# Performance work log

Measured on AMD Instinct MI355X. Metric: run time of the kernel, lower is better.

Reference implementation:

```python
import jax, jax.numpy as jnp
import numpy as np


def setup_inputs() -> dict:
    key = jax.random.key(0)
    kq, kk, kv = jax.random.split(key, 3)
    B, L, S, H, E = 2, 2048, 2048, 8, 64
    queries = jax.random.normal(kq, (B, L, H, E), dtype=jnp.float32)
    keys = jax.random.normal(kk, (B, S, H, E), dtype=jnp.float32)
    values = jax.random.normal(kv, (B, S, H, E), dtype=jnp.float32)
    a1 = jnp.float32(1.0)
    a2 = jnp.float32(1.0)
    return {"queries": queries, "keys": keys, "values": values, "a1": a1, "a2": a2}


def reference(queries, keys, values, a1, a2):
    # queries: (B,L,H,E); keys/values: (B,S,H,E)
    E = queries.shape[-1]
    scale = 1.0 / jnp.sqrt(jnp.float32(E))
    # shared QK scores: (B,H,L,S)
    qk = jnp.einsum('blhe,bshe->bhls', queries, keys) * scale
    # sparse branch: relu^2 (dropout = identity in eval)
    ssa = jnp.square(jax.nn.relu(qk))
    ssa_out = jnp.einsum('bhls,bshd->blhd', ssa, values)
    # dense branch: softmax over keys
    dsa = jax.nn.softmax(qk, axis=-1)
    dsa_out = jnp.einsum('bhls,bshd->blhd', dsa, values)
    w1 = jnp.exp(a1)
    w2 = jnp.exp(a2)
    alpha1 = w1 / (w1 + w2)
    alpha2 = w2 / (w1 + w2)
    return alpha1 * ssa_out + alpha2 * dsa_out
```

## Files before the change

### kernel.cpp

```cpp
#include <hip/hip_runtime.h>

typedef short short4v __attribute__((ext_vector_type(4)));
typedef short short8v __attribute__((ext_vector_type(8)));
typedef float float4v __attribute__((ext_vector_type(4)));
typedef unsigned short u16;

#define NB 2
#define NL 2048
#define NS 2048
#define NH 8
#define NE 64
#define HE (NH*NE)
#define NLT (NL/64)
#define NST (NS/64)
#define TILE_U16 4096

static __device__ __forceinline__ unsigned pk2bf(float a, float b) {
  union { float f; unsigned u; } x, y; x.f = a; y.f = b;
  return __builtin_amdgcn_perm(y.u + 0x8000u, x.u + 0x8000u, 0x07060302u);
}

#define GLD16(gp, lp) __builtin_amdgcn_global_load_lds( \
    (const __attribute__((address_space(1))) void*)(gp), \
    (__attribute__((address_space(3))) void*)(lp), 16, 0, 0)

static __device__ __forceinline__ int fK(int s) { return (s & 3) | ((s >> 1) & 4); }

__global__ __launch_bounds__(256)
void prepack(const float* __restrict__ kp, const float* __restrict__ vp,
             u16* __restrict__ kimg, u16* __restrict__ vimg)
{
  __shared__ __align__(16) u16 ldsv[TILE_U16];

  const int bid  = blockIdx.x;
  const int tile = bid >> 1;
  const int doV  = bid & 1;
  const int st = tile & (NST - 1);
  const int bh = tile >> 5;
  const int h  = bh & (NH - 1);
  const int b  = bh >> 3;
  const int s0 = st * 64;
  const size_t base = (size_t)b * NS * HE + h * NE;
  const int tid  = threadIdx.x;
  const int wv   = tid >> 6;
  const int lane = tid & 63;
  const int ln7  = lane & 7;

  if (!doV) {
    u16* kt = kimg + (size_t)tile * TILE_U16;
    for (int slot = tid; slot < 512; slot += 256) {
      const int srow = slot >> 3, p = slot & 7, c = p ^ fK(srow);
      const float* src = kp + base + (size_t)(s0 + srow) * HE + c * 8;
      float4 x0 = *(const float4*)src;
      float4 x1 = *(const float4*)(src + 4);
      unsigned d[4] = { pk2bf(x0.x, x0.y), pk2bf(x0.z, x0.w),
                        pk2bf(x1.x, x1.y), pk2bf(x1.z, x1.w) };
      *(int4*)(kt + slot * 8) = *(const int4*)d;
    }
    return;
  }

  u16* vt = vimg + (size_t)tile * TILE_U16;
  {
    const float* vcol = vp + base + (size_t)(s0 + wv * 16) * HE + lane;
    unsigned vr[8];
    #pragma unroll
    for (int jj = 0; jj < 8; ++jj)
      vr[jj] = pk2bf(vcol[(size_t)(2 * jj) * HE], vcol[(size_t)(2 * jj + 1) * HE]);
    #pragma unroll
    for (int i = 0; i < 2; ++i) {
      const int cs = (2 * wv + i) ^ ln7;
      int4 t4 = make_int4((int)vr[4*i+0], (int)vr[4*i+1],
                          (int)vr[4*i+2], (int)vr[4*i+3]);
      *(int4*)(&ldsv[lane * 64 + cs * 8]) = t4;
    }
  }
  __syncthreads();
  {
    const int4* s = (const int4*)ldsv;
    int4* dst = (int4*)vt;
    dst[tid]       = s[tid];
    dst[tid + 256] = s[tid + 256];
  }
}

__global__ __launch_bounds__(256, 2)
void assa_fwd(const float* __restrict__ qp, const u16* __restrict__ kimg,
              const u16* __restrict__ vimg, const float* __restrict__ a1p,
              const float* __restrict__ a2p, float* __restrict__ op)
{
  __shared__ __align__(16) u16 ldsb[2][2 * TILE_U16];

  const int tid  = threadIdx.x;
  const int wv   = tid >> 6;
  const int lane = tid & 63;
  const int ln15 = lane & 15;
  const int ln7  = lane & 7;
  const int quad = lane >> 4;

  const int bid = blockIdx.x;
  const int bh  = bid & 15;
  const int lt  = bid >> 4;
  const int h   = bh & (NH - 1);
  const int b   = bh >> 3;

  const int lbase = lt * 64 + wv * 16;

  short8v qf0, qf1;
  {
    const float* qrow = qp + ((size_t)(b * NL + lbase + ln15)) * HE + h * NE + quad * 8;
    float4 q0 = *(const float4*)(qrow);
    float4 q1 = *(const float4*)(qrow + 4);
    float4 q2 = *(const float4*)(qrow + 32);
    float4 q3 = *(const float4*)(qrow + 36);
    unsigned d0[4] = { pk2bf(0.125f*q0.x, 0.125f*q0.y), pk2bf(0.125f*q0.z, 0.125f*q0.w),
                       pk2bf(0.125f*q1.x, 0.125f*q1.y), pk2bf(0.125f*q1.z, 0.125f*q1.w) };
    unsigned d1[4] = { pk2bf(0.125f*q2.x, 0.125f*q2.y), pk2bf(0.125f*q2.z, 0.125f*q2.w),
                       pk2bf(0.125f*q3.x, 0.125f*q3.y), pk2bf(0.125f*q3.z, 0.125f*q3.w) };
    qf0 = *(const short8v*)d0;
    qf1 = *(const short8v*)d1;
  }

  short8v ones8;
  #pragma unroll
  for (int j = 0; j < 8; ++j) ones8[j] = (short)0x3F80;

  const size_t tbase = (size_t)bh * NST;

  float4v acc_s[4], acc_d[4], acc_l;
  #pragma unroll
  for (int t = 0; t < 4; ++t)
    #pragma unroll
    for (int r = 0; r < 4; ++r) { acc_s[t][r] = 0.0f; acc_d[t][r] = 0.0f; }
  #pragma unroll
  for (int r = 0; r < 4; ++r) acc_l[r] = 0.0f;

  auto dma_tile = [&](int st, int nb) {
    const int hf = wv & 1;
    const u16* g;
    u16* l;
    if (wv < 2) {
      g = kimg + (tbase + st) * TILE_U16 + hf * 2048 + lane * 8;
      l = &ldsb[nb][hf * 2048];
    } else {
      g = vimg + (tbase + st) * TILE_U16 + hf * 2048 + lane * 8;
      l = &ldsb[nb][TILE_U16 + hf * 2048];
    }
    GLD16(g,        l);
    GLD16(g +  512, l +  512);
    GLD16(g + 1024, l + 1024);
    GLD16(g + 1536, l + 1536);
  };

  dma_tile(0, 0);

  const int rperm = 8 * (ln15 >> 2) + (ln15 & 3);
  const int fk    = (ln15 & 3) | (((ln15 >> 2) & 1) << 2);

  for (int st = 0; st < NST; ++st) {
    __builtin_amdgcn_s_waitcnt(0);
    __syncthreads();
    if (st + 1 < NST) dma_tile(st + 1, (st + 1) & 1);

    const u16* kb_l = ldsb[st & 1];
    const u16* vb_l = ldsb[st & 1] + TILE_U16;

    #pragma unroll
    for (int U = 0; U < 2; ++U) {
      float4v sa0, sa1;
      #pragma unroll
      for (int r = 0; r < 4; ++r) { sa0[r] = 0.0f; sa1[r] = 0.0f; }
      const u16* krow0 = &kb_l[(32 * U + rperm) * 64];
      const u16* krow1 = krow0 + 4 * 64;
      short8v kf00 = *(const short8v*)(krow0 + (quad ^ fk) * 8);
      short8v kf01 = *(const short8v*)(krow0 + ((4 + quad) ^ fk) * 8);
      short8v kf10 = *(const short8v*)(krow1 + (quad ^ fk) * 8);
      short8v kf11 = *(const short8v*)(krow1 + ((4 + quad) ^ fk) * 8);
      sa0 = __builtin_amdgcn_mfma_f32_16x16x32_bf16(kf00, qf0, sa0, 0, 0, 0);
      sa0 = __builtin_amdgcn_mfma_f32_16x16x32_bf16(kf01, qf1, sa0, 0, 0, 0);
      sa1 = __builtin_amdgcn_mfma_f32_16x16x32_bf16(kf10, qf0, sa1, 0, 0, 0);
      sa1 = __builtin_amdgcn_mfma_f32_16x16x32_bf16(kf11, qf1, sa1, 0, 0, 0);

      float ps[8], pd[8];
      #pragma unroll
      for (int r = 0; r < 4; ++r) {
        float s0 = sa0[r], s1 = sa1[r];
        float r0 = s0 > 0.0f ? s0 : 0.0f;
        float r1 = s1 > 0.0f ? s1 : 0.0f;
        ps[r] = r0 * r0;  ps[4 + r] = r1 * r1;
        pd[r] = __expf(s0); pd[4 + r] = __expf(s1);
      }
      unsigned da[4] = { pk2bf(ps[0], ps[1]), pk2bf(ps[2], ps[3]),
                         pk2bf(ps[4], ps[5]), pk2bf(ps[6], ps[7]) };
      unsigned db[4] = { pk2bf(pd[0], pd[1]), pk2bf(pd[2], pd[3]),
                         pk2bf(pd[4], pd[5]), pk2bf(pd[6], pd[7]) };
      short8v as8 = *(const short8v*)da;
      short8v ad8 = *(const short8v*)db;

      acc_l = __builtin_amdgcn_mfma_f32_16x16x32_bf16(ad8, ones8, acc_l, 0, 0, 0);

      #pragma unroll
      for (int t = 0; t < 4; ++t) {
        short8v vf = *(const short8v*)(&vb_l[(t * 16 + ln15) * 64 +
                        (((4 * U + quad) ^ ln7) * 8)]);
        acc_s[t] = __builtin_amdgcn_mfma_f32_16x16x32_bf16(as8, vf, acc_s[t], 0, 0, 0);
        acc_d[t] = __builtin_amdgcn_mfma_f32_16x16x32_bf16(ad8, vf, acc_d[t], 0, 0, 0);
      }
    }
  }

  const float w1 = __expf(a1p[0]), w2 = __expf(a2p[0]);
  const float al1 = w1 / (w1 + w2);
  const float al2 = w2 / (w1 + w2);

  float c_d[4];
  #pragma unroll
  for (int r = 0; r < 4; ++r) c_d[r] = al2 / acc_l[r];

  #pragma unroll
  for (int t = 0; t < 4; ++t) {
    #pragma unroll
    for (int r = 0; r < 4; ++r) {
      float val = al1 * acc_s[t][r] + c_d[r] * acc_d[t][r];
      const int l = lbase + quad * 4 + r;
      const int e = t * 16 + ln15;
      op[((size_t)(b * NL + l)) * HE + h * NE + e] = val;
    }
  }
}

extern "C" void kernel_launch(void* const* d_in, const int* in_sizes, int n_in,
                              void* d_out, int out_size, void* d_ws, size_t ws_size,
                              hipStream_t stream) {
  const float* q  = (const float*)d_in[0];
  const float* k  = (const float*)d_in[1];
  const float* v  = (const float*)d_in[2];
  const float* a1 = (const float*)d_in[3];
  const float* a2 = (const float*)d_in[4];
  float* out = (float*)d_out;
  (void)in_sizes; (void)n_in; (void)out_size; (void)ws_size;

  u16* kimg = (u16*)d_ws;
  u16* vimg = kimg + (size_t)NB * NH * NST * TILE_U16;

  prepack<<<dim3(NB * NH * NST * 2), dim3(256), 0, stream>>>(k, v, kimg, vimg);
  assa_fwd<<<dim3(NB * NH * NLT), dim3(256), 0, stream>>>(q, kimg, vimg, a1, a2, out);
}
```

Before: 111.7 us.

## Fuse K/V bf16 conversion into attention kernel, drop prepack pass

Removes the separate prepack kernel that converted K and V to swizzled bf16 images in workspace. The main kernel now loads fp32 K/V directly into registers one tile ahead, converts and writes them (V transposed) into single-buffered LDS each iteration. This saves a kernel launch and the workspace write/read round trip. In exchange, every L-tile block re-reads and re-converts fp32 K/V (twice the bytes of bf16). The loop also gains an extra barrier and strided scalar V loads, replacing the async global-to-LDS DMA double buffering.

Result: slower. 115.4 us (+3.4%).

```diff
diff --git a/kernel.cpp b/kernel.cpp
--- a/kernel.cpp
+++ b/kernel.cpp
@@ -13,83 +13,21 @@
 #define HE (NH*NE)
 #define NLT (NL/64)
 #define NST (NS/64)
-#define TILE_U16 4096
 
 static __device__ __forceinline__ unsigned pk2bf(float a, float b) {
   union { float f; unsigned u; } x, y; x.f = a; y.f = b;
   return __builtin_amdgcn_perm(y.u + 0x8000u, x.u + 0x8000u, 0x07060302u);
 }
 
-#define GLD16(gp, lp) __builtin_amdgcn_global_load_lds( \
-    (const __attribute__((address_space(1))) void*)(gp), \
-    (__attribute__((address_space(3))) void*)(lp), 16, 0, 0)
-
 static __device__ __forceinline__ int fK(int s) { return (s & 3) | ((s >> 1) & 4); }
 
-__global__ __launch_bounds__(256)
-void prepack(const float* __restrict__ kp, const float* __restrict__ vp,
-             u16* __restrict__ kimg, u16* __restrict__ vimg)
-{
-  __shared__ __align__(16) u16 ldsv[TILE_U16];
-
-  const int bid  = blockIdx.x;
-  const int tile = bid >> 1;
-  const int doV  = bid & 1;
-  const int st = tile & (NST - 1);
-  const int bh = tile >> 5;
-  const int h  = bh & (NH - 1);
-  const int b  = bh >> 3;
-  const int s0 = st * 64;
-  const size_t base = (size_t)b * NS * HE + h * NE;
-  const int tid  = threadIdx.x;
-  const int wv   = tid >> 6;
-  const int lane = tid & 63;
-  const int ln7  = lane & 7;
-
-  if (!doV) {
-    u16* kt = kimg + (size_t)tile * TILE_U16;
-    for (int slot = tid; slot < 512; slot += 256) {
-      const int srow = slot >> 3, p = slot & 7, c = p ^ fK(srow);
-      const float* src = kp + base + (size_t)(s0 + srow) * HE + c * 8;
-      float4 x0 = *(const float4*)src;
-      float4 x1 = *(const float4*)(src + 4);
-      unsigned d[4] = { pk2bf(x0.x, x0.y), pk2bf(x0.z, x0.w),
-                        pk2bf(x1.x, x1.y), pk2bf(x1.z, x1.w) };
-      *(int4*)(kt + slot * 8) = *(const int4*)d;
-    }
-    return;
-  }
-
-  u16* vt = vimg + (size_t)tile * TILE_U16;
-  {
-    const float* vcol = vp + base + (size_t)(s0 + wv * 16) * HE + lane;
-    unsigned vr[8];
-    #pragma unroll
-    for (int jj = 0; jj < 8; ++jj)
-      vr[jj] = pk2bf(vcol[(size_t)(2 * jj) * HE], vcol[(size_t)(2 * jj + 1) * HE]);
-    #pragma unroll
-    for (int i = 0; i < 2; ++i) {
-      const int cs = (2 * wv + i) ^ ln7;
-      int4 t4 = make_int4((int)vr[4*i+0], (int)vr[4*i+1],
-                          (int)vr[4*i+2], (int)vr[4*i+3]);
-      *(int4*)(&ldsv[lane * 64 + cs * 8]) = t4;
-    }
-  }
-  __syncthreads();
-  {
-    const int4* s = (const int4*)ldsv;
-    int4* dst = (int4*)vt;
-    dst[tid]       = s[tid];
-    dst[tid + 256] = s[tid + 256];
-  }
-}
-
 __global__ __launch_bounds__(256, 2)
-void assa_fwd(const float* __restrict__ qp, const u16* __restrict__ kimg,
-              const u16* __restrict__ vimg, const float* __restrict__ a1p,
+void assa_fwd(const float* __restrict__ qp, const float* __restrict__ kp,
+              const float* __restrict__ vp, const float* __restrict__ a1p,
               const float* __restrict__ a2p, float* __restrict__ op)
 {
-  __shared__ __align__(16) u16 ldsb[2][2 * TILE_U16];
+  __shared__ __align__(16) u16 lds_k[64 * 64];
+  __shared__ __align__(16) u16 lds_vt[64 * 64];
 
   const int tid  = threadIdx.x;
   const int wv   = tid >> 6;
@@ -125,7 +63,30 @@
   #pragma unroll
   for (int j = 0; j < 8; ++j) ones8[j] = (short)0x3F80;
 
-  const size_t tbase = (size_t)bh * NST;
+  const size_t kvb = (size_t)b * NS * HE + h * NE;
+  const float* kb = kp + kvb;
+  const float* vb = vp + kvb;
+
+  const int rsub = lane >> 3;
+  const int kc0  = ln7 ^ (rsub & 3);
+  const int kc1  = ln7 ^ ((rsub & 3) | 4);
+  const int ksrow0 = wv * 16 + rsub;
+  const int ksrow1 = ksrow0 + 8;
+  const float* vpl = vb + (size_t)(wv * 16) * HE + lane;
+
+  float4 kpre[4];
+  float  vpre[16];
+
+  {
+    const float* k0 = kb + (size_t)ksrow0 * HE + kc0 * 8;
+    const float* k1 = kb + (size_t)ksrow1 * HE + kc1 * 8;
+    kpre[0] = *(const float4*)(k0);
+    kpre[1] = *(const float4*)(k0 + 4);
+    kpre[2] = *(const float4*)(k1);
+    kpre[3] = *(const float4*)(k1 + 4);
+    #pragma unroll
+    for (int jj = 0; jj < 16; ++jj) vpre[jj] = vpl[(size_t)jj * HE];
+  }
 
   float4v acc_s[4], acc_d[4], acc_l;
   #pragma unroll
@@ -134,43 +95,48 @@
     for (int r = 0; r < 4; ++r) { acc_s[t][r] = 0.0f; acc_d[t][r] = 0.0f; }
   #pragma unroll
   for (int r = 0; r < 4; ++r) acc_l[r] = 0.0f;
-
-  auto dma_tile = [&](int st, int nb) {
-    const int hf = wv & 1;
-    const u16* g;
-    u16* l;
-    if (wv < 2) {
-      g = kimg + (tbase + st) * TILE_U16 + hf * 2048 + lane * 8;
-      l = &ldsb[nb][hf * 2048];
-    } else {
-      g = vimg + (tbase + st) * TILE_U16 + hf * 2048 + lane * 8;
-      l = &ldsb[nb][TILE_U16 + hf * 2048];
-    }
-    GLD16(g,        l);
-    GLD16(g +  512, l +  512);
-    GLD16(g + 1024, l + 1024);
-    GLD16(g + 1536, l + 1536);
-  };
-
-  dma_tile(0, 0);
 
   const int rperm = 8 * (ln15 >> 2) + (ln15 & 3);
   const int fk    = (ln15 & 3) | (((ln15 >> 2) & 1) << 2);
 
   for (int st = 0; st < NST; ++st) {
-    __builtin_amdgcn_s_waitcnt(0);
     __syncthreads();
-    if (st + 1 < NST) dma_tile(st + 1, (st + 1) & 1);
-
-    const u16* kb_l = ldsb[st & 1];
-    const u16* vb_l = ldsb[st & 1] + TILE_U16;
+
+    {
+      unsigned kd0[4] = { pk2bf(kpre[0].x, kpre[0].y), pk2bf(kpre[0].z, kpre[0].w),
+                          pk2bf(kpre[1].x, kpre[1].y), pk2bf(kpre[1].z, kpre[1].w) };
+      unsigned kd1[4] = { pk2bf(kpre[2].x, kpre[2].y), pk2bf(kpre[2].z, kpre[2].w),
+                          pk2bf(kpre[3].x, kpre[3].y), pk2bf(kpre[3].z, kpre[3].w) };
+      *(int4*)(&lds_k[ksrow0 * 64 + ln7 * 8]) = *(const int4*)kd0;
+      *(int4*)(&lds_k[ksrow1 * 64 + ln7 * 8]) = *(const int4*)kd1;
+      #pragma unroll
+      for (int i = 0; i < 2; ++i) {
+        const int cs = (2 * wv + i) ^ ln7;
+        unsigned vd[4] = { pk2bf(vpre[8*i+0], vpre[8*i+1]), pk2bf(vpre[8*i+2], vpre[8*i+3]),
+                           pk2bf(vpre[8*i+4], vpre[8*i+5]), pk2bf(vpre[8*i+6], vpre[8*i+7]) };
+        *(int4*)(&lds_vt[lane * 64 + cs * 8]) = *(const int4*)vd;
+      }
+    }
+    __syncthreads();
+
+    if (st + 1 < NST) {
+      const float* k0 = kb + (size_t)((st + 1) * 64 + ksrow0) * HE + kc0 * 8;
+      const float* k1 = kb + (size_t)((st + 1) * 64 + ksrow1) * HE + kc1 * 8;
+      kpre[0] = *(const float4*)(k0);
+      kpre[1] = *(const float4*)(k0 + 4);
+      kpre[2] = *(const float4*)(k1);
+      kpre[3] = *(const float4*)(k1 + 4);
+      const float* vn = vpl + (size_t)(st + 1) * 64 * HE;
+      #pragma unroll
+      for (int jj = 0; jj < 16; ++jj) vpre[jj] = vn[(size_t)jj * HE];
+    }
 
     #pragma unroll
     for (int U = 0; U < 2; ++U) {
       float4v sa0, sa1;
       #pragma unroll
       for (int r = 0; r < 4; ++r) { sa0[r] = 0.0f; sa1[r] = 0.0f; }
-      const u16* krow0 = &kb_l[(32 * U + rperm) * 64];
+      const u16* krow0 = &lds_k[(32 * U + rperm) * 64];
       const u16* krow1 = krow0 + 4 * 64;
       short8v kf00 = *(const short8v*)(krow0 + (quad ^ fk) * 8);
       short8v kf01 = *(const short8v*)(krow0 + ((4 + quad) ^ fk) * 8);
@@ -201,7 +167,7 @@
 
       #pragma unroll
       for (int t = 0; t < 4; ++t) {
-        short8v vf = *(const short8v*)(&vb_l[(t * 16 + ln15) * 64 +
+        short8v vf = *(const short8v*)(&lds_vt[(t * 16 + ln15) * 64 +
                         (((4 * U + quad) ^ ln7) * 8)]);
         acc_s[t] = __builtin_amdgcn_mfma_f32_16x16x32_bf16(as8, vf, acc_s[t], 0, 0, 0);
         acc_d[t] = __builtin_amdgcn_mfma_f32_16x16x32_bf16(ad8, vf, acc_d[t], 0, 0, 0);
@@ -238,11 +204,7 @@
   const float* a1 = (const float*)d_in[3];
   const float* a2 = (const float*)d_in[4];
   float* out = (float*)d_out;
-  (void)in_sizes; (void)n_in; (void)out_size; (void)ws_size;
-
-  u16* kimg = (u16*)d_ws;
-  u16* vimg = kimg + (size_t)NB * NH * NST * TILE_U16;
-
-  prepack<<<dim3(NB * NH * NST * 2), dim3(256), 0, stream>>>(k, v, kimg, vimg);
-  assa_fwd<<<dim3(NB * NH * NLT), dim3(256), 0, stream>>>(q, kimg, vimg, a1, a2, out);
+  (void)in_sizes; (void)n_in; (void)out_size; (void)d_ws; (void)ws_size;
+
+  assa_fwd<<<dim3(NB * NH * NLT), dim3(256), 0, stream>>>(q, k, v, a1, a2, out);
 }
```

## Split key dimension across four blocks with bf16 partials and reduce kernel

Applied to the files above, without the earlier changes.

Splits the key/value sequence into four chunks, so each attention block handles only a quarter of the key tiles. This raises the grid from 512 to 2048 blocks and fills more of the GPU's CUs. Each block writes packed bf16 partial sums for the relu² and exp branches, plus row-sum partials, and a new reduce kernel combines them and applies the mixing weights. The cost is an extra launch, extra global traffic for the partials, and bf16 rounding of the partial accumulators.

Measured after the change: 118.6 us. 1.06x slower.

```diff
diff --git a/kernel.cpp b/kernel.cpp
--- a/kernel.cpp
+++ b/kernel.cpp
@@ -4,6 +4,7 @@
 typedef short short8v __attribute__((ext_vector_type(8)));
 typedef float float4v __attribute__((ext_vector_type(4)));
 typedef unsigned short u16;
+typedef unsigned int u32;
 
 #define NB 2
 #define NL 2048
@@ -14,10 +15,19 @@
 #define NLT (NL/64)
 #define NST (NS/64)
 #define TILE_U16 4096
-
-static __device__ __forceinline__ unsigned pk2bf(float a, float b) {
-  union { float f; unsigned u; } x, y; x.f = a; y.f = b;
+#define NQ 4
+#define QTILES (NST/NQ)
+#define PQ ((size_t)16*32*64*64)
+
+static __device__ __forceinline__ u32 pk2bf(float a, float b) {
+  union { float f; u32 u; } x, y; x.f = a; y.f = b;
   return __builtin_amdgcn_perm(y.u + 0x8000u, x.u + 0x8000u, 0x07060302u);
+}
+static __device__ __forceinline__ float bf_lo(u32 u) {
+  union { u32 u; float f; } v; v.u = u << 16; return v.f;
+}
+static __device__ __forceinline__ float bf_hi(u32 u) {
+  union { u32 u; float f; } v; v.u = u & 0xFFFF0000u; return v.f;
 }
 
 #define GLD16(gp, lp) __builtin_amdgcn_global_load_lds( \
@@ -53,8 +63,8 @@
       const float* src = kp + base + (size_t)(s0 + srow) * HE + c * 8;
       float4 x0 = *(const float4*)src;
       float4 x1 = *(const float4*)(src + 4);
-      unsigned d[4] = { pk2bf(x0.x, x0.y), pk2bf(x0.z, x0.w),
-                        pk2bf(x1.x, x1.y), pk2bf(x1.z, x1.w) };
+      u32 d[4] = { pk2bf(x0.x, x0.y), pk2bf(x0.z, x0.w),
+                   pk2bf(x1.x, x1.y), pk2bf(x1.z, x1.w) };
       *(int4*)(kt + slot * 8) = *(const int4*)d;
     }
     return;
@@ -63,7 +73,7 @@
   u16* vt = vimg + (size_t)tile * TILE_U16;
   {
     const float* vcol = vp + base + (size_t)(s0 + wv * 16) * HE + lane;
-    unsigned vr[8];
+    u32 vr[8];
     #pragma unroll
     for (int jj = 0; jj < 8; ++jj)
       vr[jj] = pk2bf(vcol[(size_t)(2 * jj) * HE], vcol[(size_t)(2 * jj + 1) * HE]);
@@ -86,8 +96,8 @@
 
 __global__ __launch_bounds__(256, 2)
 void assa_fwd(const float* __restrict__ qp, const u16* __restrict__ kimg,
-              const u16* __restrict__ vimg, const float* __restrict__ a1p,
-              const float* __restrict__ a2p, float* __restrict__ op)
+              const u16* __restrict__ vimg, u32* __restrict__ Ppart,
+              float* __restrict__ Lpart)
 {
   __shared__ __align__(16) u16 ldsb[2][2 * TILE_U16];
 
@@ -100,7 +110,8 @@
 
   const int bid = blockIdx.x;
   const int bh  = bid & 15;
-  const int lt  = bid >> 4;
+  const int lt  = (bid >> 4) & 31;
+  const int qt  = bid >> 9;
   const int h   = bh & (NH - 1);
   const int b   = bh >> 3;
 
@@ -113,10 +124,10 @@
     float4 q1 = *(const float4*)(qrow + 4);
     float4 q2 = *(const float4*)(qrow + 32);
     float4 q3 = *(const float4*)(qrow + 36);
-    unsigned d0[4] = { pk2bf(0.125f*q0.x, 0.125f*q0.y), pk2bf(0.125f*q0.z, 0.125f*q0.w),
-                       pk2bf(0.125f*q1.x, 0.125f*q1.y), pk2bf(0.125f*q1.z, 0.125f*q1.w) };
-    unsigned d1[4] = { pk2bf(0.125f*q2.x, 0.125f*q2.y), pk2bf(0.125f*q2.z, 0.125f*q2.w),
-                       pk2bf(0.125f*q3.x, 0.125f*q3.y), pk2bf(0.125f*q3.z, 0.125f*q3.w) };
+    u32 d0[4] = { pk2bf(0.125f*q0.x, 0.125f*q0.y), pk2bf(0.125f*q0.z, 0.125f*q0.w),
+                  pk2bf(0.125f*q1.x, 0.125f*q1.y), pk2bf(0.125f*q1.z, 0.125f*q1.w) };
+    u32 d1[4] = { pk2bf(0.125f*q2.x, 0.125f*q2.y), pk2bf(0.125f*q2.z, 0.125f*q2.w),
+                  pk2bf(0.125f*q3.x, 0.125f*q3.y), pk2bf(0.125f*q3.z, 0.125f*q3.w) };
     qf0 = *(const short8v*)d0;
     qf1 = *(const short8v*)d1;
   }
@@ -125,7 +136,7 @@
   #pragma unroll
   for (int j = 0; j < 8; ++j) ones8[j] = (short)0x3F80;
 
-  const size_t tbase = (size_t)bh * NST;
+  const size_t tbase = (size_t)bh * NST + (size_t)qt * QTILES;
 
   float4v acc_s[4], acc_d[4], acc_l;
   #pragma unroll
@@ -135,15 +146,15 @@
   #pragma unroll
   for (int r = 0; r < 4; ++r) acc_l[r] = 0.0f;
 
-  auto dma_tile = [&](int st, int nb) {
+  auto dma_tile = [&](int ti, int nb) {
     const int hf = wv & 1;
     const u16* g;
     u16* l;
     if (wv < 2) {
-      g = kimg + (tbase + st) * TILE_U16 + hf * 2048 + lane * 8;
+      g = kimg + (tbase + ti) * TILE_U16 + hf * 2048 + lane * 8;
       l = &ldsb[nb][hf * 2048];
     } else {
-      g = vimg + (tbase + st) * TILE_U16 + hf * 2048 + lane * 8;
+      g = vimg + (tbase + ti) * TILE_U16 + hf * 2048 + lane * 8;
       l = &ldsb[nb][TILE_U16 + hf * 2048];
     }
     GLD16(g,        l);
@@ -157,13 +168,13 @@
   const int rperm = 8 * (ln15 >> 2) + (ln15 & 3);
   const int fk    = (ln15 & 3) | (((ln15 >> 2) & 1) << 2);
 
-  for (int st = 0; st < NST; ++st) {
+  for (int ti = 0; ti < QTILES; ++ti) {
     __builtin_amdgcn_s_waitcnt(0);
     __syncthreads();
-    if (st + 1 < NST) dma_tile(st + 1, (st + 1) & 1);
-
-    const u16* kb_l = ldsb[st & 1];
-    const u16* vb_l = ldsb[st & 1] + TILE_U16;
+    if (ti + 1 < QTILES) dma_tile(ti + 1, (ti + 1) & 1);
+
+    const u16* kb_l = ldsb[ti & 1];
+    const u16* vb_l = ldsb[ti & 1] + TILE_U16;
 
     #pragma unroll
     for (int U = 0; U < 2; ++U) {
@@ -190,10 +201,10 @@
         ps[r] = r0 * r0;  ps[4 + r] = r1 * r1;
         pd[r] = __expf(s0); pd[4 + r] = __expf(s1);
       }
-      unsigned da[4] = { pk2bf(ps[0], ps[1]), pk2bf(ps[2], ps[3]),
-                         pk2bf(ps[4], ps[5]), pk2bf(ps[6], ps[7]) };
-      unsigned db[4] = { pk2bf(pd[0], pd[1]), pk2bf(pd[2], pd[3]),
-                         pk2bf(pd[4], pd[5]), pk2bf(pd[6], pd[7]) };
+      u32 da[4] = { pk2bf(ps[0], ps[1]), pk2bf(ps[2], ps[3]),
+                    pk2bf(ps[4], ps[5]), pk2bf(ps[6], ps[7]) };
+      u32 db[4] = { pk2bf(pd[0], pd[1]), pk2bf(pd[2], pd[3]),
+                    pk2bf(pd[4], pd[5]), pk2bf(pd[6], pd[7]) };
       short8v as8 = *(const short8v*)da;
       short8v ad8 = *(const short8v*)db;
 
@@ -209,24 +220,64 @@
     }
   }
 
+  u32* Pb = Ppart + (size_t)qt * PQ + (((size_t)bh * 32 + lt) * 64) * 64;
+  #pragma unroll
+  for (int t = 0; t < 4; ++t) {
+    #pragma unroll
+    for (int r = 0; r < 4; ++r) {
+      const int ll = wv * 16 + quad * 4 + r;
+      const int e  = t * 16 + ln15;
+      Pb[ll * 64 + e] = pk2bf(acc_s[t][r], acc_d[t][r]);
+    }
+  }
+  if (ln15 == 0) {
+    #pragma unroll
+    for (int r = 0; r < 4; ++r)
+      Lpart[(size_t)(qt * 16 + bh) * NL + lbase + quad * 4 + r] = acc_l[r];
+  }
+}
+
+__global__ __launch_bounds__(256)
+void assa_reduce(const u32* __restrict__ Ppart, const float* __restrict__ Lpart,
+                 const float* __restrict__ a1p, const float* __restrict__ a2p,
+                 float* __restrict__ op)
+{
+  const int bid  = blockIdx.x;
+  const int bh   = bid & 15;
+  const int rest = bid >> 4;
+  const int lt   = rest & 31;
+  const int seg  = rest >> 5;
+  const int tid  = threadIdx.x;
+  const int ll   = seg * 16 + (tid >> 4);
+  const int e0   = (tid & 15) * 4;
+  const int h = bh & 7, b = bh >> 3;
+  const int l = lt * 64 + ll;
+
+  const size_t pb = (((size_t)bh * 32 + lt) * 64 + ll) * 64 + e0;
+
+  float sA[4] = {0.f, 0.f, 0.f, 0.f};
+  float sD[4] = {0.f, 0.f, 0.f, 0.f};
+  float ltot = 0.0f;
+  #pragma unroll
+  for (int q = 0; q < NQ; ++q) {
+    int4 p4 = *(const int4*)(Ppart + (size_t)q * PQ + pb);
+    sA[0] += bf_lo((u32)p4.x); sD[0] += bf_hi((u32)p4.x);
+    sA[1] += bf_lo((u32)p4.y); sD[1] += bf_hi((u32)p4.y);
+    sA[2] += bf_lo((u32)p4.z); sD[2] += bf_hi((u32)p4.z);
+    sA[3] += bf_lo((u32)p4.w); sD[3] += bf_hi((u32)p4.w);
+    ltot += Lpart[(size_t)(q * 16 + bh) * NL + l];
+  }
+
   const float w1 = __expf(a1p[0]), w2 = __expf(a2p[0]);
   const float al1 = w1 / (w1 + w2);
-  const float al2 = w2 / (w1 + w2);
-
-  float c_d[4];
-  #pragma unroll
-  for (int r = 0; r < 4; ++r) c_d[r] = al2 / acc_l[r];
-
-  #pragma unroll
-  for (int t = 0; t < 4; ++t) {
-    #pragma unroll
-    for (int r = 0; r < 4; ++r) {
-      float val = al1 * acc_s[t][r] + c_d[r] * acc_d[t][r];
-      const int l = lbase + quad * 4 + r;
-      const int e = t * 16 + ln15;
-      op[((size_t)(b * NL + l)) * HE + h * NE + e] = val;
-    }
-  }
+  const float al2d = (w2 / (w1 + w2)) / ltot;
+
+  float4 o;
+  o.x = al1 * sA[0] + al2d * sD[0];
+  o.y = al1 * sA[1] + al2d * sD[1];
+  o.z = al1 * sA[2] + al2d * sD[2];
+  o.w = al1 * sA[3] + al2d * sD[3];
+  *(float4*)(op + ((size_t)(b * NL + l)) * HE + h * NE + e0) = o;
 }
 
 extern "C" void kernel_launch(void* const* d_in, const int* in_sizes, int n_in,
@@ -242,7 +293,11 @@
 
   u16* kimg = (u16*)d_ws;
   u16* vimg = kimg + (size_t)NB * NH * NST * TILE_U16;
+  u32* Ppart = (u32*)(vimg + (size_t)NB * NH * NST * TILE_U16);
+  float* Lpart = (float*)(Ppart + (size_t)NQ * PQ);
 
   prepack<<<dim3(NB * NH * NST * 2), dim3(256), 0, stream>>>(k, v, kimg, vimg);
-  assa_fwd<<<dim3(NB * NH * NLT), dim3(256), 0, stream>>>(q, kimg, vimg, a1, a2, out);
-}
+  assa_fwd<<<dim3(NB * NH * NLT * NQ), dim3(256), 0, stream>>>(q, kimg, vimg,
+                                                               Ppart, Lpart);
+  assa_reduce<<<dim3(2048), dim3(256), 0, stream>>>(Ppart, Lpart, a1, a2, out);
+}
```
